# Kernel tuning notes

Hardware: AMD Instinct MI355X
Metric: run time of the kernel (lower is better)

The kernel has to match this reference:

```python
import jax, jax.numpy as jnp
import numpy as np

FP8_MAX = 448.0  # torch.finfo(torch.float8_e4m3fn).max
FP8_MIN = -448.0
EPS = 1e-12


def fp8_quantize(x):
    """Scalar (per-tensor) dynamic fp8 e4m3 quantization, matching fp8_quantize(scalar=True).
    Returns fp8-rounded values (stored as float32) and the reciprocal scale (float32)."""
    amax = jnp.clip(jnp.max(jnp.abs(x)), EPS, None)
    scale = FP8_MAX / amax
    q = jnp.clip(x * scale, FP8_MIN, FP8_MAX)
    q = q.astype(jnp.float8_e4m3fn).astype(jnp.float32)  # rounding to fp8 grid
    return q, (1.0 / scale).astype(jnp.float32)


def setup_inputs() -> dict:
    key = jax.random.key(0)
    k_in, k_w, k_b = jax.random.split(key, 3)
    M, K, N = 16384, 2048, 2048
    input = jax.random.normal(k_in, (M, K), dtype=jnp.float32)
    weight = jax.random.normal(k_w, (N, K), dtype=jnp.float32) * 0.02
    # from_unquant: quantize weight once at init
    qweight, w_scale = fp8_quantize(weight)
    bias = jax.random.normal(k_b, (N,), dtype=jnp.float32) * 0.01
    return {"input": input, "qweight": qweight, "w_scale": w_scale, "bias": bias}


def reference(input, qweight, w_scale, bias):
    # dynamic per-tensor fp8 quantization of the activation
    qinput, a_scale = fp8_quantize(input)  # [M, K], scalar
    # torch._scaled_mm(qinput, qweight.t(), scale_a, scale_b, bias):
    #   out = (A_fp8 @ B_fp8) * scale_a * scale_b + bias, in out_dtype
    out = jnp.matmul(qinput, qweight.T)  # [M, N]
    out = out * (a_scale * w_scale) + bias[None, :]
    return out.astype(jnp.float32)
```

## Files before the change

### kernel.cpp

```cpp
#include <hip/hip_runtime.h>

typedef float f32x4 __attribute__((ext_vector_type(4)));
typedef int   i32x4 __attribute__((ext_vector_type(4)));
typedef int   i32x8 __attribute__((ext_vector_type(8)));

#define FP8MAX 448.0f


__global__ void amax_part(const float4* __restrict__ x, float* __restrict__ partial, int n4) {
    float m = 0.0f;
    int stride = gridDim.x * blockDim.x;
    for (int i = blockIdx.x * blockDim.x + threadIdx.x; i < n4; i += stride) {
        float4 v = x[i];
        m = fmaxf(m, fmaxf(fmaxf(fabsf(v.x), fabsf(v.y)), fmaxf(fabsf(v.z), fabsf(v.w))));
    }
#pragma unroll
    for (int off = 32; off > 0; off >>= 1)
        m = fmaxf(m, __shfl_down(m, off, 64));
    __shared__ float ws[4];
    int wave = threadIdx.x >> 6;
    if ((threadIdx.x & 63) == 0) ws[wave] = m;
    __syncthreads();
    if (threadIdx.x == 0)
        partial[blockIdx.x] = fmaxf(fmaxf(ws[0], ws[1]), fmaxf(ws[2], ws[3]));
}

__global__ void amax_final(const float* __restrict__ partial, unsigned* __restrict__ amax_bits, int n) {
    float m = 0.0f;
    for (int i = threadIdx.x; i < n; i += blockDim.x) m = fmaxf(m, partial[i]);
#pragma unroll
    for (int off = 32; off > 0; off >>= 1)
        m = fmaxf(m, __shfl_down(m, off, 64));
    __shared__ float ws[4];
    int wave = threadIdx.x >> 6;
    if ((threadIdx.x & 63) == 0) ws[wave] = m;
    __syncthreads();
    if (threadIdx.x == 0)
        *amax_bits = __float_as_uint(fmaxf(fmaxf(ws[0], ws[1]), fmaxf(ws[2], ws[3])));
}


__device__ __forceinline__ unsigned pack_fp8_clip(float4 v, float s) {
    float a = fminf(fmaxf(v.x * s, -FP8MAX), FP8MAX);
    float b = fminf(fmaxf(v.y * s, -FP8MAX), FP8MAX);
    float c = fminf(fmaxf(v.z * s, -FP8MAX), FP8MAX);
    float d = fminf(fmaxf(v.w * s, -FP8MAX), FP8MAX);
    int r = __builtin_amdgcn_cvt_pk_fp8_f32(a, b, 0, false);
    r = __builtin_amdgcn_cvt_pk_fp8_f32(c, d, r, true);
    return (unsigned)r;
}

__global__ void quant_act(const float4* __restrict__ x, uint4* __restrict__ q,
                          const unsigned* __restrict__ amax_bits, int n16) {
    int i = blockIdx.x * blockDim.x + threadIdx.x;
    if (i >= n16) return;
    float amax = fmaxf(__uint_as_float(*amax_bits), 1e-12f);
    float s = FP8MAX / amax;
    uint4 r;
    r.x = pack_fp8_clip(x[i * 4 + 0], s);
    r.y = pack_fp8_clip(x[i * 4 + 1], s);
    r.z = pack_fp8_clip(x[i * 4 + 2], s);
    r.w = pack_fp8_clip(x[i * 4 + 3], s);
    q[i] = r;
}

__global__ void quant_wgt(const float4* __restrict__ x, uint4* __restrict__ q, int n16) {
    int i = blockIdx.x * blockDim.x + threadIdx.x;
    if (i >= n16) return;
    uint4 r;
    float4 v0 = x[i * 4 + 0], v1 = x[i * 4 + 1], v2 = x[i * 4 + 2], v3 = x[i * 4 + 3];
    int a = __builtin_amdgcn_cvt_pk_fp8_f32(v0.x, v0.y, 0, false);
    r.x = (unsigned)__builtin_amdgcn_cvt_pk_fp8_f32(v0.z, v0.w, a, true);
    a = __builtin_amdgcn_cvt_pk_fp8_f32(v1.x, v1.y, 0, false);
    r.y = (unsigned)__builtin_amdgcn_cvt_pk_fp8_f32(v1.z, v1.w, a, true);
    a = __builtin_amdgcn_cvt_pk_fp8_f32(v2.x, v2.y, 0, false);
    r.z = (unsigned)__builtin_amdgcn_cvt_pk_fp8_f32(v2.z, v2.w, a, true);
    a = __builtin_amdgcn_cvt_pk_fp8_f32(v3.x, v3.y, 0, false);
    r.w = (unsigned)__builtin_amdgcn_cvt_pk_fp8_f32(v3.z, v3.w, a, true);
    q[i] = r;
}


__global__ __launch_bounds__(256) void gemm_fp8_mx(
    const unsigned char* __restrict__ Aq,
    const unsigned char* __restrict__ Bq,
    const unsigned* __restrict__ amax_bits,
    const float* __restrict__ w_scale_p,
    const float* __restrict__ bias,
    float* __restrict__ C,
    int M, int N, int K) {
    __shared__ unsigned char lA[128 * 128];
    __shared__ unsigned char lB[128 * 128];

    const int tid = threadIdx.x;
    const int lane = tid & 63;
    const int wave = tid >> 6;

    const int bn = blockIdx.x;
    const int bm = blockIdx.y;
    const int row0 = bm * 128;
    const int col0 = bn * 128;

    const int wm = wave >> 1;
    const int wn = wave & 1;
    const int m_base = wm * 64;
    const int n_base = wn * 64;

    const int lane_lo = lane & 15;
    const int h = lane >> 4;
    const int c0 = 2 * h;
    const int c1 = 2 * h + 1;

    f32x4 acc[4][4];
#pragma unroll
    for (int i = 0; i < 4; ++i)
#pragma unroll
        for (int j = 0; j < 4; ++j)
            acc[i][j] = (f32x4){0.f, 0.f, 0.f, 0.f};

    union frag8 { i32x8 v; i32x4 half[2]; };

    for (int k0 = 0; k0 < K; k0 += 128) {
#pragma unroll
        for (int it = 0; it < 4; ++it) {
            int chunk = tid + it * 256;
            int r = chunk >> 3;
            int cpos = chunk & 7;
            int csrc = cpos ^ (r & 7);
            const unsigned char* gA = Aq + (size_t)(row0 + r) * K + (k0 + csrc * 16);
            const unsigned char* gB = Bq + (size_t)(col0 + r) * K + (k0 + csrc * 16);
            __builtin_amdgcn_global_load_lds(
                (const __attribute__((address_space(1))) void*)gA,
                (__attribute__((address_space(3))) void*)(lA + chunk * 16), 16, 0, 0);
            __builtin_amdgcn_global_load_lds(
                (const __attribute__((address_space(1))) void*)gB,
                (__attribute__((address_space(3))) void*)(lB + chunk * 16), 16, 0, 0);
        }
        __syncthreads();

        frag8 af[4], bf[4];
#pragma unroll
        for (int i = 0; i < 4; ++i) {
            int m = m_base + i * 16 + lane_lo;
            int p0 = c0 ^ (m & 7);
            int p1 = c1 ^ (m & 7);
            af[i].half[0] = *(const i32x4*)(lA + m * 128 + p0 * 16);
            af[i].half[1] = *(const i32x4*)(lA + m * 128 + p1 * 16);
        }
#pragma unroll
        for (int j = 0; j < 4; ++j) {
            int n = n_base + j * 16 + lane_lo;
            int p0 = c0 ^ (n & 7);
            int p1 = c1 ^ (n & 7);
            bf[j].half[0] = *(const i32x4*)(lB + n * 128 + p0 * 16);
            bf[j].half[1] = *(const i32x4*)(lB + n * 128 + p1 * 16);
        }
#pragma unroll
        for (int i = 0; i < 4; ++i)
#pragma unroll
            for (int j = 0; j < 4; ++j)
                acc[i][j] = __builtin_amdgcn_mfma_scale_f32_16x16x128_f8f6f4(
                    af[i].v, bf[j].v, acc[i][j],
                    0, 0,
                    0, 0x7F7F7F7F,
                    0, 0x7F7F7F7F);
        __syncthreads();
    }

    float amax = fmaxf(__uint_as_float(*amax_bits), 1e-12f);
    float scale = FP8MAX / amax;
    float a_scale = 1.0f / scale;
    float s = a_scale * w_scale_p[0];

    const int lane_hi = lane >> 4;
#pragma unroll
    for (int i = 0; i < 4; ++i) {
#pragma unroll
        for (int j = 0; j < 4; ++j) {
            int col = col0 + n_base + j * 16 + lane_lo;
            float bv = bias[col];
#pragma unroll
            for (int r = 0; r < 4; ++r) {
                int row = row0 + m_base + i * 16 + lane_hi * 4 + r;
                C[(size_t)row * N + col] = acc[i][j][r] * s + bv;
            }
        }
    }
}


extern "C" void kernel_launch(void* const* d_in, const int* in_sizes, int n_in,
                              void* d_out, int out_size, void* d_ws, size_t ws_size,
                              hipStream_t stream) {
    const float* input   = (const float*)d_in[0];
    const float* qweight = (const float*)d_in[1];
    const float* w_scale = (const float*)d_in[2];
    const float* bias    = (const float*)d_in[3];
    float* out = (float*)d_out;

    const int N = in_sizes[3];
    const int K = in_sizes[1] / N;
    const int M = in_sizes[0] / K;

    unsigned* amax_bits = (unsigned*)d_ws;
    float* partial = (float*)((char*)d_ws + 256);
    unsigned char* qA = (unsigned char*)d_ws + 16384;
    unsigned char* qW = qA + (size_t)M * K;

    const int AMAX_BLOCKS = 2048;
    const int n4a = (M / 4) * K;
    hipLaunchKernelGGL(amax_part, dim3(AMAX_BLOCKS), dim3(256), 0, stream,
                       (const float4*)input, partial, n4a);
    hipLaunchKernelGGL(amax_final, dim3(1), dim3(256), 0, stream,
                       partial, amax_bits, AMAX_BLOCKS);

    const int n16a = n4a / 4;
    hipLaunchKernelGGL(quant_act, dim3((n16a + 255) / 256), dim3(256), 0, stream,
                       (const float4*)input, (uint4*)qA, amax_bits, n16a);

    const int n16w = (N / 4) * K / 4;
    hipLaunchKernelGGL(quant_wgt, dim3((n16w + 255) / 256), dim3(256), 0, stream,
                       (const float4*)qweight, (uint4*)qW, n16w);

    hipLaunchKernelGGL(gemm_fp8_mx, dim3(N / 128, M / 128), dim3(256), 0, stream,
                       qA, qW, amax_bits, w_scale, bias, out, M, N, K);
}
```

Measured before the change: 337.5 us.

## Fuse weight quantization into amax pass and fold final reduction into quant

```diff
diff --git a/kernel.cpp b/kernel.cpp
--- a/kernel.cpp
+++ b/kernel.cpp
@@ -5,40 +5,68 @@
 typedef int   i32x8 __attribute__((ext_vector_type(8)));
 
 #define FP8MAX 448.0f
-
-
-__global__ void amax_part(const float4* __restrict__ x, float* __restrict__ partial, int n4) {
+#define AMAX_BLOCKS 2048
+#define WQ_BLOCKS 512
+
+
+__device__ __forceinline__ unsigned pack_fp8_exact(float4 v) {
+    int r = __builtin_amdgcn_cvt_pk_fp8_f32(v.x, v.y, 0, false);
+    return (unsigned)__builtin_amdgcn_cvt_pk_fp8_f32(v.z, v.w, r, true);
+}
+
+__global__ __launch_bounds__(256) void amax_and_wquant(
+    const float4* __restrict__ x, float* __restrict__ partial, int n4,
+    const float4* __restrict__ w, uint4* __restrict__ qw, int n16w) {
+    if (blockIdx.x < AMAX_BLOCKS) {
+        float m0 = 0.0f, m1 = 0.0f;
+        int stride = AMAX_BLOCKS * 256;
+        int i = blockIdx.x * 256 + threadIdx.x;
+        for (; i + stride < n4; i += 2 * stride) {
+            float4 a = x[i];
+            float4 b = x[i + stride];
+            m0 = fmaxf(m0, fmaxf(fmaxf(fabsf(a.x), fabsf(a.y)), fmaxf(fabsf(a.z), fabsf(a.w))));
+            m1 = fmaxf(m1, fmaxf(fmaxf(fabsf(b.x), fabsf(b.y)), fmaxf(fabsf(b.z), fabsf(b.w))));
+        }
+        if (i < n4) {
+            float4 a = x[i];
+            m0 = fmaxf(m0, fmaxf(fmaxf(fabsf(a.x), fabsf(a.y)), fmaxf(fabsf(a.z), fabsf(a.w))));
+        }
+        float m = fmaxf(m0, m1);
+#pragma unroll
+        for (int off = 32; off > 0; off >>= 1)
+            m = fmaxf(m, __shfl_down(m, off, 64));
+        __shared__ float ws[4];
+        if ((threadIdx.x & 63) == 0) ws[threadIdx.x >> 6] = m;
+        __syncthreads();
+        if (threadIdx.x == 0)
+            partial[blockIdx.x] = fmaxf(fmaxf(ws[0], ws[1]), fmaxf(ws[2], ws[3]));
+    } else {
+        int stride = WQ_BLOCKS * 256;
+        for (int i = (blockIdx.x - AMAX_BLOCKS) * 256 + threadIdx.x; i < n16w; i += stride) {
+            uint4 r;
+            r.x = pack_fp8_exact(w[i * 4 + 0]);
+            r.y = pack_fp8_exact(w[i * 4 + 1]);
+            r.z = pack_fp8_exact(w[i * 4 + 2]);
+            r.w = pack_fp8_exact(w[i * 4 + 3]);
+            qw[i] = r;
+        }
+    }
+}
+
+
+__device__ __forceinline__ float reduce_partials(const float* __restrict__ partial) {
     float m = 0.0f;
-    int stride = gridDim.x * blockDim.x;
-    for (int i = blockIdx.x * blockDim.x + threadIdx.x; i < n4; i += stride) {
-        float4 v = x[i];
-        m = fmaxf(m, fmaxf(fmaxf(fabsf(v.x), fabsf(v.y)), fmaxf(fabsf(v.z), fabsf(v.w))));
-    }
+#pragma unroll
+    for (int j = 0; j < AMAX_BLOCKS / 256; ++j)
+        m = fmaxf(m, partial[threadIdx.x + j * 256]);
 #pragma unroll
     for (int off = 32; off > 0; off >>= 1)
         m = fmaxf(m, __shfl_down(m, off, 64));
     __shared__ float ws[4];
-    int wave = threadIdx.x >> 6;
-    if ((threadIdx.x & 63) == 0) ws[wave] = m;
+    if ((threadIdx.x & 63) == 0) ws[threadIdx.x >> 6] = m;
     __syncthreads();
-    if (threadIdx.x == 0)
-        partial[blockIdx.x] = fmaxf(fmaxf(ws[0], ws[1]), fmaxf(ws[2], ws[3]));
-}
-
-__global__ void amax_final(const float* __restrict__ partial, unsigned* __restrict__ amax_bits, int n) {
-    float m = 0.0f;
-    for (int i = threadIdx.x; i < n; i += blockDim.x) m = fmaxf(m, partial[i]);
-#pragma unroll
-    for (int off = 32; off > 0; off >>= 1)
-        m = fmaxf(m, __shfl_down(m, off, 64));
-    __shared__ float ws[4];
-    int wave = threadIdx.x >> 6;
-    if ((threadIdx.x & 63) == 0) ws[wave] = m;
-    __syncthreads();
-    if (threadIdx.x == 0)
-        *amax_bits = __float_as_uint(fmaxf(fmaxf(ws[0], ws[1]), fmaxf(ws[2], ws[3])));
-}
-
+    return fmaxf(fmaxf(ws[0], ws[1]), fmaxf(ws[2], ws[3]));
+}
 
 __device__ __forceinline__ unsigned pack_fp8_clip(float4 v, float s) {
     float a = fminf(fmaxf(v.x * s, -FP8MAX), FP8MAX);
@@ -50,33 +78,20 @@
     return (unsigned)r;
 }
 
-__global__ void quant_act(const float4* __restrict__ x, uint4* __restrict__ q,
-                          const unsigned* __restrict__ amax_bits, int n16) {
+__global__ __launch_bounds__(256) void quant_act(
+    const float4* __restrict__ x, uint4* __restrict__ q,
+    const float* __restrict__ partial, unsigned* __restrict__ amax_bits, int n16) {
+    float amax = fmaxf(reduce_partials(partial), 1e-12f);
+    if (blockIdx.x == 0 && threadIdx.x == 0)
+        *amax_bits = __float_as_uint(amax);
+    float s = FP8MAX / amax;
     int i = blockIdx.x * blockDim.x + threadIdx.x;
     if (i >= n16) return;
-    float amax = fmaxf(__uint_as_float(*amax_bits), 1e-12f);
-    float s = FP8MAX / amax;
     uint4 r;
     r.x = pack_fp8_clip(x[i * 4 + 0], s);
     r.y = pack_fp8_clip(x[i * 4 + 1], s);
     r.z = pack_fp8_clip(x[i * 4 + 2], s);
     r.w = pack_fp8_clip(x[i * 4 + 3], s);
-    q[i] = r;
-}
-
-__global__ void quant_wgt(const float4* __restrict__ x, uint4* __restrict__ q, int n16) {
-    int i = blockIdx.x * blockDim.x + threadIdx.x;
-    if (i >= n16) return;
-    uint4 r;
-    float4 v0 = x[i * 4 + 0], v1 = x[i * 4 + 1], v2 = x[i * 4 + 2], v3 = x[i * 4 + 3];
-    int a = __builtin_amdgcn_cvt_pk_fp8_f32(v0.x, v0.y, 0, false);
-    r.x = (unsigned)__builtin_amdgcn_cvt_pk_fp8_f32(v0.z, v0.w, a, true);
-    a = __builtin_amdgcn_cvt_pk_fp8_f32(v1.x, v1.y, 0, false);
-    r.y = (unsigned)__builtin_amdgcn_cvt_pk_fp8_f32(v1.z, v1.w, a, true);
-    a = __builtin_amdgcn_cvt_pk_fp8_f32(v2.x, v2.y, 0, false);
-    r.z = (unsigned)__builtin_amdgcn_cvt_pk_fp8_f32(v2.z, v2.w, a, true);
-    a = __builtin_amdgcn_cvt_pk_fp8_f32(v3.x, v3.y, 0, false);
-    r.w = (unsigned)__builtin_amdgcn_cvt_pk_fp8_f32(v3.z, v3.w, a, true);
     q[i] = r;
 }
 
@@ -207,20 +222,15 @@
     unsigned char* qA = (unsigned char*)d_ws + 16384;
     unsigned char* qW = qA + (size_t)M * K;
 
-    const int AMAX_BLOCKS = 2048;
-    const int n4a = (M / 4) * K;
-    hipLaunchKernelGGL(amax_part, dim3(AMAX_BLOCKS), dim3(256), 0, stream,
-                       (const float4*)input, partial, n4a);
-    hipLaunchKernelGGL(amax_final, dim3(1), dim3(256), 0, stream,
-                       partial, amax_bits, AMAX_BLOCKS);
+    const int n4a  = (M / 4) * K;
+    const int n16w = (N / 4) * K / 4;
+    hipLaunchKernelGGL(amax_and_wquant, dim3(AMAX_BLOCKS + WQ_BLOCKS), dim3(256), 0, stream,
+                       (const float4*)input, partial, n4a,
+                       (const float4*)qweight, (uint4*)qW, n16w);
 
     const int n16a = n4a / 4;
     hipLaunchKernelGGL(quant_act, dim3((n16a + 255) / 256), dim3(256), 0, stream,
-                       (const float4*)input, (uint4*)qA, amax_bits, n16a);
-
-    const int n16w = (N / 4) * K / 4;
-    hipLaunchKernelGGL(quant_wgt, dim3((n16w + 255) / 256), dim3(256), 0, stream,
-                       (const float4*)qweight, (uint4*)qW, n16w);
+                       (const float4*)input, (uint4*)qA, partial, amax_bits, n16a);
 
     hipLaunchKernelGGL(gemm_fp8_mx, dim3(N / 128, M / 128), dim3(256), 0, stream,
                        qA, qW, amax_bits, w_scale, bias, out, M, N, K);
```

Result: faster. 329.8 us (-2.3%).
